# Kernel optimization log

Measured on AMD Instinct MI355X. Metric: run time of the kernel, lower is better.

The kernel has to match this reference:

```python
import jax, jax.numpy as jnp
import numpy as np

B, T, DIN, H, HB = 256, 512, 64, 256, 128  # batch, seq, input, hidden, bi-hidden


def rnn_layer(x, wih, whh, bih, bhh):
    # PyTorch nn.RNN (tanh) layer, batch_first. x: [B,T,I] -> [B,T,H]
    xw = jnp.einsum('bti,hi->bth', x, wih) + bih
    h0 = jnp.zeros((x.shape[0], whh.shape[0]), x.dtype)
    def step(h, xt):
        h = jnp.tanh(xt + h @ whh.T + bhh)
        return h, h
    _, ys = jax.lax.scan(step, h0, jnp.swapaxes(xw, 0, 1))
    return jnp.swapaxes(ys, 0, 1)


def gru_layer(x, wih, whh, bih, bhh, reverse=False):
    # PyTorch nn.GRU layer (gate order r,z,n). x: [B,T,I] -> [B,T,Hh]
    Hh = whh.shape[1]
    xg = jnp.einsum('bti,gi->btg', x, wih) + bih  # [B,T,3Hh]
    h0 = jnp.zeros((x.shape[0], Hh), x.dtype)
    def step(h, xt):
        hg = h @ whh.T + bhh
        xr, xz, xn = jnp.split(xt, 3, axis=-1)
        hr, hz, hn = jnp.split(hg, 3, axis=-1)
        r = jax.nn.sigmoid(xr + hr)
        z = jax.nn.sigmoid(xz + hz)
        n = jnp.tanh(xn + r * hn)
        h = (1.0 - z) * n + z * h
        return h, h
    _, ys = jax.lax.scan(step, h0, jnp.swapaxes(xg, 0, 1), reverse=reverse)
    return jnp.swapaxes(ys, 0, 1)


def setup_inputs() -> dict:
    key = jax.random.key(0)
    ks = iter(jax.random.split(key, 40))
    s = 0.05
    def w(shape):
        return jax.random.normal(next(ks), shape, jnp.float32) * s
    inp = {"x": jax.random.normal(next(ks), (B, T, DIN), jnp.float32)}
    inp.update(dict(
        rnn_wih0=w((H, DIN)), rnn_whh0=w((H, H)), rnn_bih0=w((H,)), rnn_bhh0=w((H,)),
        rnn_wih1=w((H, H)), rnn_whh1=w((H, H)), rnn_bih1=w((H,)), rnn_bhh1=w((H,)),
        gru_wih=w((2, 3 * H, H)), gru_whh=w((2, 3 * H, H)),
        gru_bih=w((2, 3 * H)), gru_bhh=w((2, 3 * H)),
        # bi-GRU: index order [l0_fwd, l0_bwd, l1_fwd, l1_bwd]; all inputs have width H
        bi_wih=w((4, 3 * HB, H)), bi_whh=w((4, 3 * HB, HB)),
        bi_bih=w((4, 3 * HB)), bi_bhh=w((4, 3 * HB)),
        att_w1=w((H // 2, H)), att_b1=w((H // 2,)), att_w2=w((1, H // 2)), att_b2=w((1,)),
        bn_gamma=jnp.ones((H,), jnp.float32), bn_beta=jnp.zeros((H,), jnp.float32),
        bn_mean=jnp.zeros((H,), jnp.float32), bn_var=jnp.ones((H,), jnp.float32),
        fc_w1=w((H // 2, H)), fc_b1=w((H // 2,)),
        fc_w2=w((H // 4, H // 2)), fc_b2=w((H // 4,)),
        fc_w3=w((1, H // 4)), fc_b3=w((1,)),
    ))
    return inp


def reference(x, rnn_wih0, rnn_whh0, rnn_bih0, rnn_bhh0,
              rnn_wih1, rnn_whh1, rnn_bih1, rnn_bhh1,
              gru_wih, gru_whh, gru_bih, gru_bhh,
              bi_wih, bi_whh, bi_bih, bi_bhh,
              att_w1, att_b1, att_w2, att_b2,
              bn_gamma, bn_beta, bn_mean, bn_var,
              fc_w1, fc_b1, fc_w2, fc_b2, fc_w3, fc_b3):
    # --- stacked tanh RNN (2 layers); dropout is identity in eval ---
    h = rnn_layer(x, rnn_wih0, rnn_whh0, rnn_bih0, rnn_bhh0)
    h = rnn_layer(h, rnn_wih1, rnn_whh1, rnn_bih1, rnn_bhh1)
    # --- stacked GRU (2 layers) ---
    for l in range(2):
        h = gru_layer(h, gru_wih[l], gru_whh[l], gru_bih[l], gru_bhh[l])
    # --- bidirectional GRU (2 layers, hidden HB per direction) ---
    for l in range(2):
        f = gru_layer(h, bi_wih[2 * l], bi_whh[2 * l], bi_bih[2 * l], bi_bhh[2 * l])
        b = gru_layer(h, bi_wih[2 * l + 1], bi_whh[2 * l + 1], bi_bih[2 * l + 1], bi_bhh[2 * l + 1], reverse=True)
        h = jnp.concatenate([f, b], axis=-1)  # [B,T,H]
    # --- additive attention pooling over time ---
    scores = jnp.tanh(h @ att_w1.T + att_b1) @ att_w2.T + att_b2  # [B,T,1]
    weights = jax.nn.softmax(scores, axis=1)
    ctx = jnp.sum(weights * h, axis=1)  # [B,H]
    # --- batchnorm (eval mode: running stats) ---
    ctx = (ctx - bn_mean) / jnp.sqrt(bn_var + 1e-5) * bn_gamma + bn_beta
    # --- FC head ---
    o = jax.nn.relu(ctx @ fc_w1.T + fc_b1)
    o = jax.nn.relu(o @ fc_w2.T + fc_b2)
    return o @ fc_w3.T + fc_b3  # [B,1]
```

## Files before the change

### kernel.cpp

```cpp
#include <hip/hip_runtime.h>


typedef short sv8 __attribute__((ext_vector_type(8)));
typedef short sv4 __attribute__((ext_vector_type(4)));
typedef short sv2 __attribute__((ext_vector_type(2)));
typedef float fv4 __attribute__((ext_vector_type(4)));
typedef float fv2 __attribute__((ext_vector_type(2)));

__device__ __forceinline__ float bf2f(short s) {
  union { unsigned u; float f; } v; v.u = ((unsigned)(unsigned short)s) << 16; return v.f;
}
__device__ __forceinline__ short f2bf(float f) {
  union { float f; unsigned u; } v; v.f = f;
  unsigned r = (v.u + 0x7fffu + ((v.u >> 16) & 1u)) >> 16;
  return (short)r;
}
__device__ __forceinline__ float sigm(float x) { return 1.f / (1.f + __expf(-x)); }
__device__ __forceinline__ float tanh_f(float x) {
  float ax = fabsf(x);
  float e = __expf(2.f * ax);
  float t = 1.f - 2.f / (e + 1.f);
  return copysignf(t, x);
}
__device__ __forceinline__ void lds_barrier() {
  asm volatile("s_waitcnt lgkmcnt(0)" ::: "memory");
  __builtin_amdgcn_s_barrier();
}

__global__ __launch_bounds__(256) void f2b4(const float* __restrict__ s,
                                            short* __restrict__ d, int n4) {
  int i = blockIdx.x * 256 + threadIdx.x;
  if (i < n4) {
    fv4 v = ((const fv4*)s)[i];
    sv4 o;
    o[0] = f2bf(v[0]); o[1] = f2bf(v[1]); o[2] = f2bf(v[2]); o[3] = f2bf(v[3]);
    ((sv4*)d)[i] = o;
  }
}

__global__ __launch_bounds__(256) void bias_prep(
    const float* __restrict__ rbih0, const float* __restrict__ rbhh0,
    const float* __restrict__ rbih1, const float* __restrict__ rbhh1,
    const float* __restrict__ gbih, const float* __restrict__ gbhh,
    const float* __restrict__ bbih, const float* __restrict__ bbhh,
    float* __restrict__ BC) {
  int i = blockIdx.x * 256 + threadIdx.x;
  if (i >= 3584) return;
  float v;
  if (i < 256)       v = rbih0[i] + rbhh0[i];
  else if (i < 512)  { int c = i - 256; v = rbih1[c] + rbhh1[c]; }
  else if (i < 2048) { int j = i - 512; int c = j % 768;
                       v = gbih[j] + (c < 512 ? gbhh[j] : 0.f); }
  else               { int j = i - 2048; int c = j % 384;
                       v = bbih[j] + (c < 256 ? bbhh[j] : 0.f); }
  BC[i] = v;
}

template <int KS, int ACT, bool AF32>
__global__ __launch_bounds__(256, 4) void gemm_xw(
    const void* __restrict__ Av, const short* __restrict__ W,
    const float* __restrict__ bias, short* __restrict__ C,
    int N, int ldc, int w0, int l2tc) {
  const int K = KS * 32;
  const int lane = threadIdx.x & 63, wv = threadIdx.x >> 6;
  const int l15 = lane & 15, q = lane >> 4;
  const int m0 = blockIdx.x * 128 + wv * 32;
  const int tcm = (1 << l2tc) - 1;

  sv8 af[2][KS];
#pragma unroll
  for (int s = 0; s < 2; ++s) {
    const int r = m0 + s * 16 + l15;
    const size_t arow = (size_t)(r >> l2tc) * 512 + w0 + (r & tcm);
    if (AF32) {
      const float* ap = (const float*)Av + arow * K + q * 8;
#pragma unroll
      for (int k = 0; k < KS; ++k) {
        fv4 lo = *(const fv4*)(ap + k * 32);
        fv4 hi = *(const fv4*)(ap + k * 32 + 4);
        sv8 o;
        o[0] = f2bf(lo[0]); o[1] = f2bf(lo[1]); o[2] = f2bf(lo[2]); o[3] = f2bf(lo[3]);
        o[4] = f2bf(hi[0]); o[5] = f2bf(hi[1]); o[6] = f2bf(hi[2]); o[7] = f2bf(hi[3]);
        af[s][k] = o;
      }
    } else {
      const short* ap = (const short*)Av + arow * K + q * 8;
#pragma unroll
      for (int k = 0; k < KS; ++k) af[s][k] = *(const sv8*)(ap + k * 32);
    }
  }
  const int N16 = N >> 4;
  for (int nt = 0; nt < N16; ++nt) {
    const short* wp = W + (size_t)(nt * 16 + l15) * K + q * 8;
    fv4 acc0 = {0.f, 0.f, 0.f, 0.f}, acc1 = {0.f, 0.f, 0.f, 0.f};
#pragma unroll
    for (int k = 0; k < KS; ++k) {
      sv8 bf = *(const sv8*)(wp + k * 32);
      acc0 = __builtin_amdgcn_mfma_f32_16x16x32_bf16(af[0][k], bf, acc0, 0, 0, 0);
      acc1 = __builtin_amdgcn_mfma_f32_16x16x32_bf16(af[1][k], bf, acc1, 0, 0, 0);
    }
    float bv = bias[nt * 16 + l15];
#pragma unroll
    for (int s = 0; s < 2; ++s) {
      fv4 a = s ? acc1 : acc0;
#pragma unroll
      for (int j = 0; j < 4; ++j) {
        float v = a[j] + bv;
        if (ACT == 1) v = tanh_f(v);
        int row = m0 + s * 16 + q * 4 + j;
        C[(size_t)row * ldc + nt * 16 + l15] = f2bf(v);
      }
    }
  }
}

__global__ __launch_bounds__(512, 2) void rnn_scan(
    const short* __restrict__ xg, const short* __restrict__ whh,
    short* __restrict__ hout, int w0, int Tc, int first,
    short* __restrict__ hst) {
  constexpr int T = 512, H = 256, NR = 8, SP = H + 8;
  __shared__ __align__(16) short hl[NR * H];
  __shared__ __align__(16) float S[NR * SP];
  const int tid = threadIdx.x, lane = tid & 63, wv = tid >> 6;
  const int l15 = lane & 15, q = lane >> 4;
  const int r0 = blockIdx.x * NR;

  sv8 wf[2][8];
#pragma unroll
  for (int s = 0; s < 2; ++s) {
    const short* wp = whh + (size_t)(wv * 32 + s * 16 + l15) * H + q * 8;
#pragma unroll
    for (int k = 0; k < 8; ++k) wf[s][k] = *(const sv8*)(wp + k * 32);
  }
  const int row = wv;
  const int c = (tid & 63) * 4;
  const size_t xbase = ((size_t)(r0 + row) * Tc) * H + c;
  const size_t obase = ((size_t)(r0 + row) * T + w0) * H + c;
  const int hlo = row * H + (c ^ (row << 3));

  sv4 hp;
  if (first) { sv4 z = {0,0,0,0}; hp = z; }
  else hp = *(const sv4*)(hst + (size_t)(r0 + row) * H + c);
  *(sv4*)&hl[hlo] = hp;
  sv4 xr = *(const sv4*)(xg + xbase);
  __syncthreads();

  const int arow = l15 & 7;
  const short* hb = hl + arow * H;
  const int asw = arow << 3;

  for (int t = 0; t < Tc; ++t) {
    sv4 pf;
    if (t + 1 < Tc) pf = *(const sv4*)(xg + xbase + (size_t)(t + 1) * H);
    fv4 acc[2] = {{0,0,0,0},{0,0,0,0}};
#pragma unroll
    for (int k = 0; k < 8; ++k) {
      sv8 a = *(const sv8*)(hb + ((k * 32 + q * 8) ^ asw));
#pragma unroll
      for (int s = 0; s < 2; ++s)
        acc[s] = __builtin_amdgcn_mfma_f32_16x16x32_bf16(a, wf[s][k], acc[s], 0, 0, 0);
    }
    if (q < 2) {
#pragma unroll
      for (int s = 0; s < 2; ++s)
#pragma unroll
        for (int j = 0; j < 4; ++j)
          S[(q * 4 + j) * SP + wv * 32 + s * 16 + l15] = acc[s][j];
    }
    lds_barrier();
    fv4 sv = *(const fv4*)&S[row * SP + c];
    sv4 o;
#pragma unroll
    for (int i = 0; i < 4; ++i) o[i] = f2bf(tanh_f(bf2f(xr[i]) + sv[i]));
    hp = o;
    *(sv4*)&hl[hlo] = o;
    *(sv4*)(hout + obase + (size_t)t * H) = o;
    xr = pf;
    lds_barrier();
  }
  *(sv4*)(hst + (size_t)(r0 + row) * H + c) = hp;
}

__global__ __launch_bounds__(512, 2) void gru_scan(
    const short* __restrict__ xg, const short* __restrict__ whh,
    const float* __restrict__ bhn, short* __restrict__ hout,
    int w0, int Tc, int first, short* __restrict__ hst) {
  constexpr int T = 512, H = 256, G = 768, NR = 8, SP = G + 8;
  __shared__ __align__(16) short hl[NR * H];
  __shared__ __align__(16) float S[NR * SP];
  const int tid = threadIdx.x, lane = tid & 63, wv = tid >> 6;
  const int l15 = lane & 15, q = lane >> 4;
  const int r0 = blockIdx.x * NR;

  sv8 wf[6][8];
#pragma unroll
  for (int s = 0; s < 6; ++s) {
    const short* wp = whh + (size_t)(wv * 96 + s * 16 + l15) * H + q * 8;
#pragma unroll
    for (int k = 0; k < 8; ++k) wf[s][k] = *(const sv8*)(wp + k * 32);
  }
  const int row = wv;
  const int c = (tid & 63) * 4;
  const size_t xbase = ((size_t)(r0 + row) * Tc) * G + c;
  const size_t obase = ((size_t)(r0 + row) * T + w0) * H + c;
  const int hlo = row * H + (c ^ (row << 3));
  fv4 bn = *(const fv4*)(bhn + c);

  sv4 hp;
  if (first) { sv4 z = {0,0,0,0}; hp = z; }
  else hp = *(const sv4*)(hst + (size_t)(r0 + row) * H + c);
  *(sv4*)&hl[hlo] = hp;
  sv4 xr0 = *(const sv4*)(xg + xbase);
  sv4 xr1 = *(const sv4*)(xg + xbase + 256);
  sv4 xr2 = *(const sv4*)(xg + xbase + 512);
  __syncthreads();

  const int arow = l15 & 7;
  const short* hb = hl + arow * H;
  const int asw = arow << 3;

  for (int t = 0; t < Tc; ++t) {
    sv4 pf0, pf1, pf2;
    if (t + 1 < Tc) {
      const size_t xb = xbase + (size_t)(t + 1) * G;
      pf0 = *(const sv4*)(xg + xb);
      pf1 = *(const sv4*)(xg + xb + 256);
      pf2 = *(const sv4*)(xg + xb + 512);
    }
    fv4 acc[6];
#pragma unroll
    for (int s = 0; s < 6; ++s) acc[s] = (fv4){0,0,0,0};
#pragma unroll
    for (int k = 0; k < 8; ++k) {
      sv8 a = *(const sv8*)(hb + ((k * 32 + q * 8) ^ asw));
#pragma unroll
      for (int s = 0; s < 6; ++s)
        acc[s] = __builtin_amdgcn_mfma_f32_16x16x32_bf16(a, wf[s][k], acc[s], 0, 0, 0);
    }
    if (q < 2) {
#pragma unroll
      for (int s = 0; s < 6; ++s)
#pragma unroll
        for (int j = 0; j < 4; ++j)
          S[(q * 4 + j) * SP + wv * 96 + s * 16 + l15] = acc[s][j];
    }
    lds_barrier();
    fv4 sr = *(const fv4*)&S[row * SP + c];
    fv4 sz = *(const fv4*)&S[row * SP + c + 256];
    fv4 sn = *(const fv4*)&S[row * SP + c + 512];
    sv4 o;
#pragma unroll
    for (int i = 0; i < 4; ++i) {
      float rr = sigm(bf2f(xr0[i]) + sr[i]);
      float zz = sigm(bf2f(xr1[i]) + sz[i]);
      float nn = tanh_f(bf2f(xr2[i]) + rr * (sn[i] + bn[i]));
      o[i] = f2bf((1.f - zz) * nn + zz * bf2f(hp[i]));
    }
    hp = o;
    *(sv4*)&hl[hlo] = o;
    *(sv4*)(hout + obase + (size_t)t * H) = o;
    xr0 = pf0; xr1 = pf1; xr2 = pf2;
    lds_barrier();
  }
  *(sv4*)(hst + (size_t)(r0 + row) * H + c) = hp;
}

__global__ __launch_bounds__(512, 2) void bigru_scan(
    const short* __restrict__ xgf, const short* __restrict__ xgb,
    const short* __restrict__ whh_f, const short* __restrict__ whh_b,
    const float* __restrict__ bhn_f, const float* __restrict__ bhn_b,
    short* __restrict__ hout, int w0f, int w0b, int Tc, int first,
    short* __restrict__ hstf, short* __restrict__ hstb) {
  constexpr int T = 512, HB = 128, GL = 384, NR = 8, SP = GL + 8, HO = 256;
  __shared__ __align__(16) short hl[NR * HB];
  __shared__ __align__(16) float S[NR * SP];
  const int tid = threadIdx.x, lane = tid & 63, wv = tid >> 6;
  const int l15 = lane & 15, q = lane >> 4;
  const int dir = blockIdx.x >> 5;
  const int r0 = (blockIdx.x & 31) * NR;
  const short* whh = dir ? whh_b : whh_f;
  const short* xg  = dir ? xgb : xgf;
  const float* bhn = dir ? bhn_b : bhn_f;
  short* hst = dir ? hstb : hstf;
  const int w0 = dir ? w0b : w0f;

  sv8 wf[3][4];
#pragma unroll
  for (int s = 0; s < 3; ++s) {
    const short* wp = whh + (size_t)(wv * 48 + s * 16 + l15) * HB + q * 8;
#pragma unroll
    for (int k = 0; k < 4; ++k) wf[s][k] = *(const sv8*)(wp + k * 32);
  }
  const int row = wv;
  const int c = (tid & 63) * 2;
  const size_t xbase = ((size_t)(r0 + row) * Tc) * GL + c;
  const size_t obase = ((size_t)(r0 + row) * T + w0) * HO + dir * HB + c;
  const int hlo = row * HB + (c ^ (row << 3));
  fv2 bn = *(const fv2*)(bhn + c);

  sv2 hp;
  if (first) { sv2 z = {0,0}; hp = z; }
  else hp = *(const sv2*)(hst + (size_t)(r0 + row) * HB + c);
  *(sv2*)&hl[hlo] = hp;
  int tl = dir ? (Tc - 1) : 0;
  sv2 xr0 = *(const sv2*)(xg + xbase + (size_t)tl * GL);
  sv2 xr1 = *(const sv2*)(xg + xbase + (size_t)tl * GL + 128);
  sv2 xr2 = *(const sv2*)(xg + xbase + (size_t)tl * GL + 256);
  __syncthreads();

  const int arow = l15 & 7;
  const short* hb = hl + arow * HB;
  const int asw = arow << 3;

  for (int t = 0; t < Tc; ++t) {
    tl = dir ? (Tc - 1 - t) : t;
    sv2 pf0, pf1, pf2;
    if (t + 1 < Tc) {
      const int tn = dir ? (Tc - 2 - t) : (t + 1);
      const size_t xb = xbase + (size_t)tn * GL;
      pf0 = *(const sv2*)(xg + xb);
      pf1 = *(const sv2*)(xg + xb + 128);
      pf2 = *(const sv2*)(xg + xb + 256);
    }
    fv4 acc[3];
#pragma unroll
    for (int s = 0; s < 3; ++s) acc[s] = (fv4){0,0,0,0};
#pragma unroll
    for (int k = 0; k < 4; ++k) {
      sv8 a = *(const sv8*)(hb + ((k * 32 + q * 8) ^ asw));
#pragma unroll
      for (int s = 0; s < 3; ++s)
        acc[s] = __builtin_amdgcn_mfma_f32_16x16x32_bf16(a, wf[s][k], acc[s], 0, 0, 0);
    }
    if (q < 2) {
#pragma unroll
      for (int s = 0; s < 3; ++s)
#pragma unroll
        for (int j = 0; j < 4; ++j)
          S[(q * 4 + j) * SP + wv * 48 + s * 16 + l15] = acc[s][j];
    }
    lds_barrier();
    fv2 sr = *(const fv2*)&S[row * SP + c];
    fv2 sz = *(const fv2*)&S[row * SP + c + 128];
    fv2 sn = *(const fv2*)&S[row * SP + c + 256];
    sv2 o;
#pragma unroll
    for (int i = 0; i < 2; ++i) {
      float rr = sigm(bf2f(xr0[i]) + sr[i]);
      float zz = sigm(bf2f(xr1[i]) + sz[i]);
      float nn = tanh_f(bf2f(xr2[i]) + rr * (sn[i] + bn[i]));
      o[i] = f2bf((1.f - zz) * nn + zz * bf2f(hp[i]));
    }
    hp = o;
    *(sv2*)&hl[hlo] = o;
    *(sv2*)(hout + obase + (size_t)tl * HO) = o;
    xr0 = pf0; xr1 = pf1; xr2 = pf2;
    lds_barrier();
  }
  *(sv2*)(hst + (size_t)(r0 + row) * HB + c) = hp;
}

__global__ __launch_bounds__(256) void att_scores(
    const short* __restrict__ s1, const float* __restrict__ w2,
    const float* __restrict__ b2, float* __restrict__ sc, int w0, int l2tc) {
  const int r = blockIdx.x * 256 + threadIdx.x;
  const int b = r >> l2tc, tl = r & ((1 << l2tc) - 1);
  const short* p = s1 + (size_t)r * 128;
  float sum = 0.f;
#pragma unroll
  for (int c = 0; c < 16; ++c) {
    sv8 v = *(const sv8*)(p + c * 8);
#pragma unroll
    for (int j = 0; j < 8; ++j) sum += bf2f(v[j]) * w2[c * 8 + j];
  }
  sc[b * 512 + w0 + tl] = sum + b2[0];
}

__global__ __launch_bounds__(256) void pool_head(
    const float* __restrict__ sc, const short* __restrict__ h,
    const float* __restrict__ bng, const float* __restrict__ bnb,
    const float* __restrict__ bnm, const float* __restrict__ bnv,
    const float* __restrict__ w1, const float* __restrict__ b1,
    const float* __restrict__ w2, const float* __restrict__ b2,
    const float* __restrict__ w3, const float* __restrict__ b3,
    float* __restrict__ out) {
  constexpr int T = 512, H = 256;
  __shared__ float wts[T];
  __shared__ float red[4];
  __shared__ float ctxs[H];
  __shared__ float o1[128];
  __shared__ float o2[64];
  const int b = blockIdx.x, tid = threadIdx.x, lane = tid & 63, wv = tid >> 6;

  float s0 = sc[b * T + tid], s1v = sc[b * T + 256 + tid];
  float m = fmaxf(s0, s1v);
#pragma unroll
  for (int o = 32; o >= 1; o >>= 1) m = fmaxf(m, __shfl_xor(m, o));
  if (lane == 0) red[wv] = m;
  __syncthreads();
  m = fmaxf(fmaxf(red[0], red[1]), fmaxf(red[2], red[3]));

  float e0 = __expf(s0 - m), e1 = __expf(s1v - m);
  wts[tid] = e0; wts[tid + 256] = e1;
  float se = e0 + e1;
#pragma unroll
  for (int o = 32; o >= 1; o >>= 1) se += __shfl_xor(se, o);
  __syncthreads();
  if (lane == 0) red[wv] = se;
  __syncthreads();
  const float Z = red[0] + red[1] + red[2] + red[3];

  float cx = 0.f;
  const short* hp = h + (size_t)b * T * H + tid;
  for (int t = 0; t < T; ++t) cx += wts[t] * bf2f(hp[(size_t)t * H]);
  cx /= Z;
  cx = (cx - bnm[tid]) * rsqrtf(bnv[tid] + 1e-5f) * bng[tid] + bnb[tid];
  ctxs[tid] = cx;
  __syncthreads();

  if (tid < 128) {
    const float* wr = w1 + tid * H;
    float a = 0.f;
#pragma unroll 8
    for (int k = 0; k < H; ++k) a += ctxs[k] * wr[k];
    o1[tid] = fmaxf(a + b1[tid], 0.f);
  }
  __syncthreads();
  if (tid < 64) {
    const float* wr = w2 + tid * 128;
    float a = 0.f;
#pragma unroll 8
    for (int k = 0; k < 128; ++k) a += o1[k] * wr[k];
    o2[tid] = fmaxf(a + b2[tid], 0.f);
  }
  __syncthreads();
  if (tid < 64) {
    float p = o2[tid] * w3[tid];
#pragma unroll
    for (int o = 32; o >= 1; o >>= 1) p += __shfl_xor(p, o);
    if (tid == 0) out[b] = p + b3[0];
  }
}

extern "C" void kernel_launch(void* const* d_in, const int* in_sizes, int n_in,
                              void* d_out, int out_size, void* d_ws, size_t ws_size,
                              hipStream_t stream) {
  const float* x_f    = (const float*)d_in[0];
  const float* rwih0  = (const float*)d_in[1];
  const float* rwhh0  = (const float*)d_in[2];
  const float* rbih0  = (const float*)d_in[3];
  const float* rbhh0  = (const float*)d_in[4];
  const float* rwih1  = (const float*)d_in[5];
  const float* rwhh1  = (const float*)d_in[6];
  const float* rbih1  = (const float*)d_in[7];
  const float* rbhh1  = (const float*)d_in[8];
  const float* gwih_f = (const float*)d_in[9];
  const float* gwhh_f = (const float*)d_in[10];
  const float* gbih   = (const float*)d_in[11];
  const float* gbhh   = (const float*)d_in[12];
  const float* bwih_f = (const float*)d_in[13];
  const float* bwhh_f = (const float*)d_in[14];
  const float* bbih   = (const float*)d_in[15];
  const float* bbhh   = (const float*)d_in[16];
  const float* aw1_f  = (const float*)d_in[17];
  const float* ab1    = (const float*)d_in[18];
  const float* aw2    = (const float*)d_in[19];
  const float* ab2    = (const float*)d_in[20];
  const float* bng    = (const float*)d_in[21];
  const float* bnb    = (const float*)d_in[22];
  const float* bnm    = (const float*)d_in[23];
  const float* bnv    = (const float*)d_in[24];
  const float* fw1    = (const float*)d_in[25];
  const float* fb1    = (const float*)d_in[26];
  const float* fw2    = (const float*)d_in[27];
  const float* fb2    = (const float*)d_in[28];
  const float* fw3    = (const float*)d_in[29];
  const float* fb3    = (const float*)d_in[30];
  (void)in_sizes; (void)n_in; (void)out_size;

  char* ws = (char*)d_ws;
  size_t off = 0;
  auto take = [&](size_t bytes) -> char* {
    char* p = ws + off;
    off += (bytes + 255) & ~(size_t)255;
    return p;
  };
  short* wih0 = (short*)take(16384 * 2);
  short* whh0 = (short*)take(65536 * 2);
  short* wih1 = (short*)take(65536 * 2);
  short* whh1 = (short*)take(65536 * 2);
  short* gwih = (short*)take(393216 * 2);
  short* gwhh = (short*)take(393216 * 2);
  short* bwih = (short*)take(393216 * 2);
  short* bwhh = (short*)take(196608 * 2);
  short* aw1  = (short*)take(32768 * 2);
  float* BC   = (float*)take(3584 * 4);
  short* hstA = (short*)take(65536 * 2);
  short* hstF = (short*)take(32768 * 2);
  short* hstB = (short*)take(32768 * 2);
  float* SC   = (float*)take(131072ull * 4);
  short* H1   = (short*)take(131072ull * 256 * 2);
  short* H2   = (short*)take(131072ull * 256 * 2);

  const size_t region = ws_size > off ? ws_size - off : 0;
  const size_t XGF = 131072ull * 768 * 2;
  int NC;
  if      (region >= XGF)      NC = 1;
  else if (region >= XGF / 2)  NC = 2;
  else if (region >= XGF / 4)  NC = 4;
  else if (region >= XGF / 8)  NC = 8;
  else if (region >= XGF / 16) NC = 16;
  else                         NC = 32;
  const int Tc = 512 / NC;
  int l2 = 0; while ((1 << l2) < Tc) ++l2;
  short* XG  = (short*)(ws + off);
  short* XGb = XG + (size_t)256 * Tc * 384;

#define CONV(src, dst, n) f2b4<<<(n) / 1024, 256, 0, stream>>>(src, dst, (n) / 4)
  CONV(rwih0, wih0, 16384);
  CONV(rwhh0, whh0, 65536);
  CONV(rwih1, wih1, 65536);
  CONV(rwhh1, whh1, 65536);
  CONV(gwih_f, gwih, 393216);
  CONV(gwhh_f, gwhh, 393216);
  CONV(bwih_f, bwih, 393216);
  CONV(bwhh_f, bwhh, 196608);
  CONV(aw1_f, aw1, 32768);
#undef CONV
  bias_prep<<<14, 256, 0, stream>>>(rbih0, rbhh0, rbih1, rbhh1,
                                    gbih, gbhh, bbih, bbhh, BC);

  const int gg = 2 * Tc;

  for (int c = 0; c < NC; ++c) {
    gemm_xw<2, 0, true><<<gg, 256, 0, stream>>>(x_f, wih0, BC, XG, 256, 256, c * Tc, l2);
    rnn_scan<<<32, 512, 0, stream>>>(XG, whh0, H1, c * Tc, Tc, c == 0, hstA);
  }
  for (int c = 0; c < NC; ++c) {
    gemm_xw<8, 0, false><<<gg, 256, 0, stream>>>(H1, wih1, BC + 256, XG, 256, 256, c * Tc, l2);
    rnn_scan<<<32, 512, 0, stream>>>(XG, whh1, H1, c * Tc, Tc, c == 0, hstA);
  }
  for (int c = 0; c < NC; ++c) {
    gemm_xw<8, 0, false><<<gg, 256, 0, stream>>>(H1, gwih, BC + 512, XG, 768, 768, c * Tc, l2);
    gru_scan<<<32, 512, 0, stream>>>(XG, gwhh, gbhh + 512, H1, c * Tc, Tc, c == 0, hstA);
  }
  for (int c = 0; c < NC; ++c) {
    gemm_xw<8, 0, false><<<gg, 256, 0, stream>>>(H1, gwih + 196608, BC + 1280, XG, 768, 768, c * Tc, l2);
    gru_scan<<<32, 512, 0, stream>>>(XG, gwhh + 196608, gbhh + 768 + 512, H1, c * Tc, Tc, c == 0, hstA);
  }
  for (int s = 0; s < NC; ++s) {
    const int w0f = s * Tc, w0b = (NC - 1 - s) * Tc;
    gemm_xw<8, 0, false><<<gg, 256, 0, stream>>>(H1, bwih, BC + 2048, XG, 384, 384, w0f, l2);
    gemm_xw<8, 0, false><<<gg, 256, 0, stream>>>(H1, bwih + 98304, BC + 2432, XGb, 384, 384, w0b, l2);
    bigru_scan<<<64, 512, 0, stream>>>(XG, XGb, bwhh, bwhh + 49152,
                                       bbhh + 256, bbhh + 384 + 256,
                                       H2, w0f, w0b, Tc, s == 0, hstF, hstB);
  }
  for (int s = 0; s < NC; ++s) {
    const int w0f = s * Tc, w0b = (NC - 1 - s) * Tc;
    gemm_xw<8, 0, false><<<gg, 256, 0, stream>>>(H2, bwih + 2 * 98304, BC + 2816, XG, 384, 384, w0f, l2);
    gemm_xw<8, 0, false><<<gg, 256, 0, stream>>>(H2, bwih + 3 * 98304, BC + 3200, XGb, 384, 384, w0b, l2);
    bigru_scan<<<64, 512, 0, stream>>>(XG, XGb, bwhh + 2 * 49152, bwhh + 3 * 49152,
                                       bbhh + 2 * 384 + 256, bbhh + 3 * 384 + 256,
                                       H1, w0f, w0b, Tc, s == 0, hstF, hstB);
  }
  for (int c = 0; c < NC; ++c) {
    gemm_xw<8, 1, false><<<gg, 256, 0, stream>>>(H1, aw1, ab1, XG, 128, 128, c * Tc, l2);
    att_scores<<<Tc, 256, 0, stream>>>(XG, aw2, ab2, SC, c * Tc, l2);
  }
  pool_head<<<256, 256, 0, stream>>>(SC, H1, bng, bnb, bnm, bnv,
                                     fw1, fb1, fw2, fb2, fw3, fb3, (float*)d_out);
}
```

Baseline: 5.872 ms.

## Halve GRU scan block to 4 waves and pin recurrent weights in AGPRs

```diff
diff --git a/kernel.cpp b/kernel.cpp
--- a/kernel.cpp
+++ b/kernel.cpp
@@ -132,6 +132,12 @@
 #pragma unroll
     for (int k = 0; k < 8; ++k) wf[s][k] = *(const sv8*)(wp + k * 32);
   }
+#pragma unroll
+  for (int s = 0; s < 2; ++s)
+#pragma unroll
+    for (int k = 0; k < 8; ++k)
+      asm volatile("" : "+a"(wf[s][k]));
+
   const int row = wv;
   const int c = (tid & 63) * 4;
   const size_t xbase = ((size_t)(r0 + row) * Tc) * H + c;
@@ -181,7 +187,7 @@
   *(sv4*)(hst + (size_t)(r0 + row) * H + c) = hp;
 }
 
-__global__ __launch_bounds__(512, 2) void gru_scan(
+__global__ __launch_bounds__(256, 1) void gru_scan(
     const short* __restrict__ xg, const short* __restrict__ whh,
     const float* __restrict__ bhn, short* __restrict__ hout,
     int w0, int Tc, int first, short* __restrict__ hst) {
@@ -192,27 +198,34 @@
   const int l15 = lane & 15, q = lane >> 4;
   const int r0 = blockIdx.x * NR;
 
-  sv8 wf[6][8];
-#pragma unroll
-  for (int s = 0; s < 6; ++s) {
-    const short* wp = whh + (size_t)(wv * 96 + s * 16 + l15) * H + q * 8;
-#pragma unroll
-    for (int k = 0; k < 8; ++k) wf[s][k] = *(const sv8*)(wp + k * 32);
-  }
-  const int row = wv;
-  const int c = (tid & 63) * 4;
+  sv8 wf[12][8];
+#pragma unroll
+  for (int ti = 0; ti < 12; ++ti) {
+    const short* wp = whh + (size_t)(wv * 192 + ti * 16 + l15) * H + q * 8;
+#pragma unroll
+    for (int k = 0; k < 8; ++k) wf[ti][k] = *(const sv8*)(wp + k * 32);
+  }
+#pragma unroll
+  for (int ti = 0; ti < 8; ++ti)
+#pragma unroll
+    for (int k = 0; k < 8; ++k)
+      asm volatile("" : "+a"(wf[ti][k]));
+
+  const int row = tid >> 5, cb = tid & 31;
+  const int c = cb * 8;
   const size_t xbase = ((size_t)(r0 + row) * Tc) * G + c;
   const size_t obase = ((size_t)(r0 + row) * T + w0) * H + c;
   const int hlo = row * H + (c ^ (row << 3));
-  fv4 bn = *(const fv4*)(bhn + c);
-
-  sv4 hp;
-  if (first) { sv4 z = {0,0,0,0}; hp = z; }
-  else hp = *(const sv4*)(hst + (size_t)(r0 + row) * H + c);
-  *(sv4*)&hl[hlo] = hp;
-  sv4 xr0 = *(const sv4*)(xg + xbase);
-  sv4 xr1 = *(const sv4*)(xg + xbase + 256);
-  sv4 xr2 = *(const sv4*)(xg + xbase + 512);
+  const float* bp = bhn + c;
+  fv4 bn0 = *(const fv4*)bp, bn1 = *(const fv4*)(bp + 4);
+
+  sv8 hp;
+  if (first) { sv8 z = {0,0,0,0,0,0,0,0}; hp = z; }
+  else hp = *(const sv8*)(hst + (size_t)(r0 + row) * H + c);
+  *(sv8*)&hl[hlo] = hp;
+  sv8 xr0 = *(const sv8*)(xg + xbase);
+  sv8 xr1 = *(const sv8*)(xg + xbase + 256);
+  sv8 xr2 = *(const sv8*)(xg + xbase + 512);
   __syncthreads();
 
   const int arow = l15 & 7;
@@ -220,49 +233,57 @@
   const int asw = arow << 3;
 
   for (int t = 0; t < Tc; ++t) {
-    sv4 pf0, pf1, pf2;
+    sv8 pf0, pf1, pf2;
     if (t + 1 < Tc) {
       const size_t xb = xbase + (size_t)(t + 1) * G;
-      pf0 = *(const sv4*)(xg + xb);
-      pf1 = *(const sv4*)(xg + xb + 256);
-      pf2 = *(const sv4*)(xg + xb + 512);
-    }
-    fv4 acc[6];
-#pragma unroll
-    for (int s = 0; s < 6; ++s) acc[s] = (fv4){0,0,0,0};
+      pf0 = *(const sv8*)(xg + xb);
+      pf1 = *(const sv8*)(xg + xb + 256);
+      pf2 = *(const sv8*)(xg + xb + 512);
+    }
+    fv4 acc[12];
+#pragma unroll
+    for (int ti = 0; ti < 12; ++ti) acc[ti] = (fv4){0,0,0,0};
 #pragma unroll
     for (int k = 0; k < 8; ++k) {
       sv8 a = *(const sv8*)(hb + ((k * 32 + q * 8) ^ asw));
 #pragma unroll
-      for (int s = 0; s < 6; ++s)
-        acc[s] = __builtin_amdgcn_mfma_f32_16x16x32_bf16(a, wf[s][k], acc[s], 0, 0, 0);
+      for (int ti = 0; ti < 12; ++ti)
+        acc[ti] = __builtin_amdgcn_mfma_f32_16x16x32_bf16(a, wf[ti][k], acc[ti], 0, 0, 0);
     }
     if (q < 2) {
 #pragma unroll
-      for (int s = 0; s < 6; ++s)
+      for (int ti = 0; ti < 12; ++ti)
 #pragma unroll
         for (int j = 0; j < 4; ++j)
-          S[(q * 4 + j) * SP + wv * 96 + s * 16 + l15] = acc[s][j];
+          S[(q * 4 + j) * SP + wv * 192 + ti * 16 + l15] = acc[ti][j];
     }
     lds_barrier();
-    fv4 sr = *(const fv4*)&S[row * SP + c];
-    fv4 sz = *(const fv4*)&S[row * SP + c + 256];
-    fv4 sn = *(const fv4*)&S[row * SP + c + 512];
-    sv4 o;
+    const float* s0 = &S[row * SP + c];
+    fv4 r0v = *(const fv4*)s0,         r1v = *(const fv4*)(s0 + 4);
+    fv4 z0v = *(const fv4*)(s0 + 256), z1v = *(const fv4*)(s0 + 260);
+    fv4 n0v = *(const fv4*)(s0 + 512), n1v = *(const fv4*)(s0 + 516);
+    sv8 o;
 #pragma unroll
     for (int i = 0; i < 4; ++i) {
-      float rr = sigm(bf2f(xr0[i]) + sr[i]);
-      float zz = sigm(bf2f(xr1[i]) + sz[i]);
-      float nn = tanh_f(bf2f(xr2[i]) + rr * (sn[i] + bn[i]));
+      float rr = sigm(bf2f(xr0[i]) + r0v[i]);
+      float zz = sigm(bf2f(xr1[i]) + z0v[i]);
+      float nn = tanh_f(bf2f(xr2[i]) + rr * (n0v[i] + bn0[i]));
       o[i] = f2bf((1.f - zz) * nn + zz * bf2f(hp[i]));
     }
+#pragma unroll
+    for (int i = 0; i < 4; ++i) {
+      float rr = sigm(bf2f(xr0[4 + i]) + r1v[i]);
+      float zz = sigm(bf2f(xr1[4 + i]) + z1v[i]);
+      float nn = tanh_f(bf2f(xr2[4 + i]) + rr * (n1v[i] + bn1[i]));
+      o[4 + i] = f2bf((1.f - zz) * nn + zz * bf2f(hp[4 + i]));
+    }
     hp = o;
-    *(sv4*)&hl[hlo] = o;
-    *(sv4*)(hout + obase + (size_t)t * H) = o;
+    *(sv8*)&hl[hlo] = o;
+    *(sv8*)(hout + obase + (size_t)t * H) = o;
     xr0 = pf0; xr1 = pf1; xr2 = pf2;
     lds_barrier();
   }
-  *(sv4*)(hst + (size_t)(r0 + row) * H + c) = hp;
+  *(sv8*)(hst + (size_t)(r0 + row) * H + c) = hp;
 }
 
 __global__ __launch_bounds__(512, 2) void bigru_scan(
@@ -291,6 +312,12 @@
 #pragma unroll
     for (int k = 0; k < 4; ++k) wf[s][k] = *(const sv8*)(wp + k * 32);
   }
+#pragma unroll
+  for (int s = 0; s < 3; ++s)
+#pragma unroll
+    for (int k = 0; k < 4; ++k)
+      asm volatile("" : "+a"(wf[s][k]));
+
   const int row = wv;
   const int c = (tid & 63) * 2;
   const size_t xbase = ((size_t)(r0 + row) * Tc) * GL + c;
@@ -542,11 +569,11 @@
   }
   for (int c = 0; c < NC; ++c) {
     gemm_xw<8, 0, false><<<gg, 256, 0, stream>>>(H1, gwih, BC + 512, XG, 768, 768, c * Tc, l2);
-    gru_scan<<<32, 512, 0, stream>>>(XG, gwhh, gbhh + 512, H1, c * Tc, Tc, c == 0, hstA);
+    gru_scan<<<32, 256, 0, stream>>>(XG, gwhh, gbhh + 512, H1, c * Tc, Tc, c == 0, hstA);
   }
   for (int c = 0; c < NC; ++c) {
     gemm_xw<8, 0, false><<<gg, 256, 0, stream>>>(H1, gwih + 196608, BC + 1280, XG, 768, 768, c * Tc, l2);
-    gru_scan<<<32, 512, 0, stream>>>(XG, gwhh + 196608, gbhh + 768 + 512, H1, c * Tc, Tc, c == 0, hstA);
+    gru_scan<<<32, 256, 0, stream>>>(XG, gwhh + 196608, gbhh + 768 + 512, H1, c * Tc, Tc, c == 0, hstA);
   }
   for (int s = 0; s < NC; ++s) {
     const int w0f = s * Tc, w0b = (NC - 1 - s) * Tc;
```

Measured after the change: 5.795 ms. No clear change (-1.3%).
